# Performance work log

Measured on AMD Instinct MI355X. Metric: run time of the kernel, lower is better.

The kernel has to match this reference:

```python
import jax, jax.numpy as jnp
import numpy as np

N = 50000          # nodes
E = 800000         # directed edges (before self-loops)
NUM_CLASSES = 10
NEG_SLOPE = 0.2    # PyG GATConv default leaky_relu slope


def segment_softmax(logits, seg, num_segments):
    # numerically stable softmax over edges grouped by target node
    m = jax.ops.segment_max(logits, seg, num_segments=num_segments)
    e = jnp.exp(logits - m[seg])
    s = jax.ops.segment_sum(e, seg, num_segments=num_segments)
    return e / s[seg]


def gat_conv(x, src, dst, W, a_src, a_dst, b, n_nodes):
    # single-head PyG-style GATConv (eval mode: attention dropout disabled)
    h = x @ W                              # [N, C]
    alpha_src = h @ a_src                  # [N]
    alpha_dst = h @ a_dst                  # [N]
    logits = jax.nn.leaky_relu(alpha_src[src] + alpha_dst[dst], NEG_SLOPE)  # [E']
    alpha = segment_softmax(logits, dst, n_nodes)                            # [E']
    out = jax.ops.segment_sum(h[src] * alpha[:, None], dst, num_segments=n_nodes)
    return out + b


def setup_inputs() -> dict:
    key = jax.random.key(0)
    ks = jax.random.split(key, 13)
    x = jax.random.normal(ks[0], (N, 11), dtype=jnp.float32)
    edge_index = jax.random.randint(ks[1], (2, E), 0, N, dtype=jnp.int32)
    batch = jnp.zeros((N,), dtype=jnp.int32)  # unused by forward (no pooling)
    s = 0.1
    W1 = jax.random.normal(ks[2], (11, 16), jnp.float32) * s
    a1_src = jax.random.normal(ks[3], (16,), jnp.float32) * s
    a1_dst = jax.random.normal(ks[4], (16,), jnp.float32) * s
    b1 = jnp.zeros((16,), jnp.float32)
    W2 = jax.random.normal(ks[5], (16, 64), jnp.float32) * s
    a2_src = jax.random.normal(ks[6], (64,), jnp.float32) * s
    a2_dst = jax.random.normal(ks[7], (64,), jnp.float32) * s
    b2 = jnp.zeros((64,), jnp.float32)
    Wl = jax.random.normal(ks[8], (64, NUM_CLASSES), jnp.float32) * s
    bl = jnp.zeros((NUM_CLASSES,), jnp.float32)
    return {"x": x, "edge_index": edge_index, "batch": batch,
            "W1": W1, "a1_src": a1_src, "a1_dst": a1_dst, "b1": b1,
            "W2": W2, "a2_src": a2_src, "a2_dst": a2_dst, "b2": b2,
            "Wl": Wl, "bl": bl}


def reference(x, edge_index, batch, W1, a1_src, a1_dst, b1,
              W2, a2_src, a2_dst, b2, Wl, bl):
    n = x.shape[0]
    loop = jnp.arange(n, dtype=edge_index.dtype)
    src = jnp.concatenate([edge_index[0], loop])  # add self-loops (PyG default)
    dst = jnp.concatenate([edge_index[1], loop])
    h = gat_conv(x, src, dst, W1, a1_src, a1_dst, b1, n)
    h = jax.nn.relu(h)
    h = gat_conv(h, src, dst, W2, a2_src, a2_dst, b2, n)
    return h @ Wl + bl
```

## Files before the change

kernel.cpp:

```cpp
#include <hip/hip_runtime.h>
#include <hip/hip_bf16.h>
#include <hip/hip_fp16.h>

#define NEG_SLOPE 0.2f
#define BUCK 128
#define BSTRIDE 4096
#define SRCM 0x1FFFFFFu
#define SCH 2048

__device__ __forceinline__ float lrelu(float x) {
    return x > 0.f ? x : NEG_SLOPE * x;
}

__global__ __launch_bounds__(256)
void front_kernel(const float* __restrict__ x,
                  const float* __restrict__ W1,
                  const float* __restrict__ a1s, const float* __restrict__ a1d,
                  __half* __restrict__ h, float* __restrict__ as, float* __restrict__ ad,
                  int n, int tb,
                  const float* __restrict__ W2,
                  const float* __restrict__ a2s, const float* __restrict__ a2d,
                  const float* __restrict__ b2,
                  const float* __restrict__ Wl, const float* __restrict__ bl,
                  float* __restrict__ va, float* __restrict__ vd,
                  float* __restrict__ Wc, float* __restrict__ bc,
                  int* __restrict__ gcur, int nbuck) {
    const int bid = blockIdx.x;
    if (bid < tb) {
        constexpr int F_IN = 11, C_OUT = 16;
        __shared__ float sW[F_IN * C_OUT];
        __shared__ float sAs[C_OUT];
        __shared__ float sAd[C_OUT];
        for (int i = threadIdx.x; i < F_IN * C_OUT; i += 256) sW[i] = W1[i];
        if (threadIdx.x < C_OUT) { sAs[threadIdx.x] = a1s[threadIdx.x]; sAd[threadIdx.x] = a1d[threadIdx.x]; }
        __syncthreads();
        int i = bid * 256 + threadIdx.x;
        if (i >= n) return;
        float xin[F_IN];
#pragma unroll
        for (int f = 0; f < F_IN; ++f) xin[f] = x[(size_t)i * F_IN + f];
        float r[C_OUT];
        float s_acc = 0.f, d_acc = 0.f;
#pragma unroll
        for (int c = 0; c < C_OUT; ++c) {
            float acc = 0.f;
#pragma unroll
            for (int f = 0; f < F_IN; ++f) acc = fmaf(xin[f], sW[f * C_OUT + c], acc);
            r[c] = acc;
            s_acc = fmaf(acc, sAs[c], s_acc);
            d_acc = fmaf(acc, sAd[c], d_acc);
        }
        unsigned int u[8];
#pragma unroll
        for (int k = 0; k < 8; ++k) {
            __half2 hh = __floats2half2_rn(r[2 * k], r[2 * k + 1]);
            u[k] = *reinterpret_cast<unsigned int*>(&hh);
        }
        uint4* hp = reinterpret_cast<uint4*>(&h[(size_t)i * 16]);
        hp[0] = make_uint4(u[0], u[1], u[2], u[3]);
        hp[1] = make_uint4(u[4], u[5], u[6], u[7]);
        as[i] = s_acc;
        ad[i] = d_acc;
    } else {
        int t = threadIdx.x;
        for (int i = t; i < nbuck; i += 256) gcur[i] = i * BSTRIDE;
        if (t < 16) {
            float s = 0.f, s2 = 0.f;
            for (int c = 0; c < 64; ++c) {
                float w = W2[t * 64 + c];
                s = fmaf(w, a2s[c], s);
                s2 = fmaf(w, a2d[c], s2);
            }
            va[t] = s; vd[t] = s2;
        }
        int i = t - 64;
        if (i >= 0 && i < 160) {
            int f = i / 10, k = i % 10;
            float s = 0.f;
            for (int c = 0; c < 64; ++c) s = fmaf(W2[f * 64 + c], Wl[c * 10 + k], s);
            Wc[i] = s;
        }
        int k2 = t - 240;
        if (k2 >= 0 && k2 < 10) {
            float s = bl[k2];
            for (int c = 0; c < 64; ++c) s = fmaf(b2[c], Wl[c * 10 + k2], s);
            bc[k2] = s;
        }
    }
}

__global__ __launch_bounds__(256)
void scatter_kernel(const int* __restrict__ ei, int E, int ET,
                    int* __restrict__ gcur, uint2* __restrict__ pk, int nbuck,
                    const float* __restrict__ as1, const float* __restrict__ ad1) {
    __shared__ int lhist[512];
    for (int i = threadIdx.x; i < nbuck; i += 256) lhist[i] = 0;
    __syncthreads();
    const int tid = threadIdx.x;
    const int beg = blockIdx.x * SCH;

    int rs0, rs1, rs2, rs3, rs4, rs5, rs6, rs7;
    int rd0, rd1, rd2, rd3, rd4, rd5, rd6, rd7;
    const int e0 = beg + tid * 4;
    const int e1 = e0 + 1024;
    if (e0 + 3 < E) {
        const int4 s4 = *reinterpret_cast<const int4*>(&ei[e0]);
        const int4 d4 = *reinterpret_cast<const int4*>(&ei[E + e0]);
        rs0 = s4.x; rs1 = s4.y; rs2 = s4.z; rs3 = s4.w;
        rd0 = d4.x; rd1 = d4.y; rd2 = d4.z; rd3 = d4.w;
    } else {
        rs0 = rd0 = (e0 + 0 < ET) ? ((e0 + 0 < E) ? 0 : e0 + 0 - E) : -1;
        if (e0 + 0 < E) { rs0 = ei[e0 + 0]; rd0 = ei[E + e0 + 0]; }
        rs1 = rd1 = (e0 + 1 < ET) ? ((e0 + 1 < E) ? 0 : e0 + 1 - E) : -1;
        if (e0 + 1 < E) { rs1 = ei[e0 + 1]; rd1 = ei[E + e0 + 1]; }
        rs2 = rd2 = (e0 + 2 < ET) ? ((e0 + 2 < E) ? 0 : e0 + 2 - E) : -1;
        if (e0 + 2 < E) { rs2 = ei[e0 + 2]; rd2 = ei[E + e0 + 2]; }
        rs3 = rd3 = (e0 + 3 < ET) ? ((e0 + 3 < E) ? 0 : e0 + 3 - E) : -1;
        if (e0 + 3 < E) { rs3 = ei[e0 + 3]; rd3 = ei[E + e0 + 3]; }
    }
    if (e1 + 3 < E) {
        const int4 s4 = *reinterpret_cast<const int4*>(&ei[e1]);
        const int4 d4 = *reinterpret_cast<const int4*>(&ei[E + e1]);
        rs4 = s4.x; rs5 = s4.y; rs6 = s4.z; rs7 = s4.w;
        rd4 = d4.x; rd5 = d4.y; rd6 = d4.z; rd7 = d4.w;
    } else {
        rs4 = rd4 = (e1 + 0 < ET) ? ((e1 + 0 < E) ? 0 : e1 + 0 - E) : -1;
        if (e1 + 0 < E) { rs4 = ei[e1 + 0]; rd4 = ei[E + e1 + 0]; }
        rs5 = rd5 = (e1 + 1 < ET) ? ((e1 + 1 < E) ? 0 : e1 + 1 - E) : -1;
        if (e1 + 1 < E) { rs5 = ei[e1 + 1]; rd5 = ei[E + e1 + 1]; }
        rs6 = rd6 = (e1 + 2 < ET) ? ((e1 + 2 < E) ? 0 : e1 + 2 - E) : -1;
        if (e1 + 2 < E) { rs6 = ei[e1 + 2]; rd6 = ei[E + e1 + 2]; }
        rs7 = rd7 = (e1 + 3 < ET) ? ((e1 + 3 < E) ? 0 : e1 + 3 - E) : -1;
        if (e1 + 3 < E) { rs7 = ei[e1 + 3]; rd7 = ei[E + e1 + 3]; }
    }

    if (rd0 >= 0) atomicAdd(&lhist[rd0 >> 7], 1);
    if (rd1 >= 0) atomicAdd(&lhist[rd1 >> 7], 1);
    if (rd2 >= 0) atomicAdd(&lhist[rd2 >> 7], 1);
    if (rd3 >= 0) atomicAdd(&lhist[rd3 >> 7], 1);
    if (rd4 >= 0) atomicAdd(&lhist[rd4 >> 7], 1);
    if (rd5 >= 0) atomicAdd(&lhist[rd5 >> 7], 1);
    if (rd6 >= 0) atomicAdd(&lhist[rd6 >> 7], 1);
    if (rd7 >= 0) atomicAdd(&lhist[rd7 >> 7], 1);
    __syncthreads();

    for (int i = threadIdx.x; i < nbuck; i += 256) {
        int c = lhist[i];
        lhist[i] = (c > 0) ? atomicAdd(&gcur[i], c) : 0;
    }
    __syncthreads();

#define EMIT(RS, RD)                                                                   \
    if (RD >= 0) {                                                                     \
        float w = __expf(lrelu(as1[RS] + ad1[RD]));                                    \
        int slot = atomicAdd(&lhist[RD >> 7], 1);                                      \
        pk[slot] = make_uint2(((unsigned int)(RD & 127) << 25) | (unsigned int)RS,     \
                              __float_as_uint(w));                                     \
    }
    EMIT(rs0, rd0) EMIT(rs1, rd1) EMIT(rs2, rd2) EMIT(rs3, rd3)
    EMIT(rs4, rd4) EMIT(rs5, rd5) EMIT(rs6, rd6) EMIT(rs7, rd7)
#undef EMIT
}

__global__ __launch_bounds__(256)
void bucketsort_kernel(const uint2* __restrict__ pk,
                       const int* __restrict__ gcur,
                       uint2* __restrict__ cw,
                       int* __restrict__ row_beg, int* __restrict__ deg,
                       int n) {
    __shared__ uint2 sbuf[BSTRIDE];
    __shared__ uint2 dbuf[BSTRIDE];
    __shared__ int lcnt[BUCK];
    __shared__ int lofs[BUCK];
    const int tid = threadIdx.x;
    const int base = blockIdx.x * BUCK;
    const int beg = blockIdx.x * BSTRIDE;
    const int cnt = gcur[blockIdx.x] - beg;

    if (tid < BUCK) lcnt[tid] = 0;
    for (int i = tid * 2; i < cnt; i += 512) {
        if (i + 1 < cnt) {
            *reinterpret_cast<uint4*>(&sbuf[i]) = *reinterpret_cast<const uint4*>(&pk[beg + i]);
        } else {
            sbuf[i] = pk[beg + i];
        }
    }
    __syncthreads();
    for (int i = tid; i < cnt; i += 256)
        atomicAdd(&lcnt[sbuf[i].x >> 25], 1);
    __syncthreads();
    int v = 0;
    if (tid < BUCK) { v = lcnt[tid]; lofs[tid] = v; }
    __syncthreads();
    for (int off = 1; off < BUCK; off <<= 1) {
        int u = 0;
        if (tid < BUCK && tid >= off) u = lofs[tid - off];
        __syncthreads();
        if (tid < BUCK && tid >= off) lofs[tid] += u;
        __syncthreads();
    }
    if (tid < BUCK) {
        int excl = lofs[tid] - v;
        if (base + tid < n) {
            row_beg[base + tid] = beg + excl;
            deg[base + tid] = v;
        }
        lcnt[tid] = excl;
    }
    __syncthreads();
    for (int i = tid; i < cnt; i += 256) {
        uint2 rec = sbuf[i];
        int slot = atomicAdd(&lcnt[rec.x >> 25], 1);
        dbuf[slot] = rec;
    }
    __syncthreads();
    for (int i = tid * 2; i < cnt; i += 512) {
        if (i + 1 < cnt) {
            *reinterpret_cast<uint4*>(&cw[beg + i]) = *reinterpret_cast<uint4*>(&dbuf[i]);
        } else {
            cw[beg + i] = dbuf[i];
        }
    }
}

__global__ void gat_agg1_kernel(const int* __restrict__ row_beg,
                                const int* __restrict__ deg,
                                const uint2* __restrict__ cw,
                                const __half* __restrict__ h,
                                const float* __restrict__ b1,
                                const float* __restrict__ va,
                                const float* __restrict__ vd,
                                __half* __restrict__ X1r,
                                float* __restrict__ as2,
                                float* __restrict__ ad2, int n) {
    __shared__ float sb1[16], sva[16], svd[16];
    if (threadIdx.x < 16) {
        sb1[threadIdx.x] = b1[threadIdx.x];
        sva[threadIdx.x] = va[threadIdx.x];
        svd[threadIdx.x] = vd[threadIdx.x];
    }
    __syncthreads();
    int node = (blockIdx.x * blockDim.x + threadIdx.x) >> 4;
    int sl = threadIdx.x & 15;
    if (node >= n) return;
    int beg = row_beg[node];
    int end = beg + deg[node];

    const int eq = sl >> 2;
    const int cl = sl & 3;
    float lsum = 0.f;
    float4 acc = {0.f, 0.f, 0.f, 0.f};
    for (int chunk = beg; chunk < end; chunk += 16) {
        int e = chunk + sl;
        float wv = 0.f; int sv = 0;
        if (e < end) {
            uint2 rec = cw[e];
            sv = (int)(rec.x & SRCM);
            wv = __uint_as_float(rec.y);
            lsum += wv;
        }
        const int nch = min(16, end - chunk);
        const int T = (nch + 3) >> 2;
        for (int t = 0; t < T; ++t) {
            int j = t * 4 + eq;
            float wj = __shfl(wv, j, 16);
            int   sj = __shfl(sv, j, 16);
            if (j < nch) {
                uint2 hv2 = *reinterpret_cast<const uint2*>(&h[(size_t)sj * 16 + cl * 4]);
                float2 f01 = __half22float2(*reinterpret_cast<__half2*>(&hv2.x));
                float2 f23 = __half22float2(*reinterpret_cast<__half2*>(&hv2.y));
                acc.x = fmaf(wj, f01.x, acc.x);
                acc.y = fmaf(wj, f01.y, acc.y);
                acc.z = fmaf(wj, f23.x, acc.z);
                acc.w = fmaf(wj, f23.y, acc.w);
            }
        }
    }
#pragma unroll
    for (int k = 1; k < 16; k <<= 1) lsum += __shfl_xor(lsum, k, 16);
#pragma unroll
    for (int k = 4; k < 16; k <<= 1) {
        acc.x += __shfl_xor(acc.x, k, 16);
        acc.y += __shfl_xor(acc.y, k, 16);
        acc.z += __shfl_xor(acc.z, k, 16);
        acc.w += __shfl_xor(acc.w, k, 16);
    }
    float inv = 1.f / lsum;
    float x0 = fmaxf(fmaf(acc.x, inv, sb1[cl * 4 + 0]), 0.f);
    float x1 = fmaxf(fmaf(acc.y, inv, sb1[cl * 4 + 1]), 0.f);
    float x2 = fmaxf(fmaf(acc.z, inv, sb1[cl * 4 + 2]), 0.f);
    float x3 = fmaxf(fmaf(acc.w, inv, sb1[cl * 4 + 3]), 0.f);
    if (eq == 0) {
        __half2 p01 = __floats2half2_rn(x0, x1);
        __half2 p23 = __floats2half2_rn(x2, x3);
        uint2 o = make_uint2(*reinterpret_cast<unsigned int*>(&p01),
                             *reinterpret_cast<unsigned int*>(&p23));
        *reinterpret_cast<uint2*>(&X1r[(size_t)node * 16 + cl * 4]) = o;
    }
    float p = x0 * sva[cl * 4] + x1 * sva[cl * 4 + 1] + x2 * sva[cl * 4 + 2] + x3 * sva[cl * 4 + 3];
    float q = x0 * svd[cl * 4] + x1 * svd[cl * 4 + 1] + x2 * svd[cl * 4 + 2] + x3 * svd[cl * 4 + 3];
    p += __shfl_xor(p, 1, 16); p += __shfl_xor(p, 2, 16);
    q += __shfl_xor(q, 1, 16); q += __shfl_xor(q, 2, 16);
    if (sl == 0) { as2[node] = p; ad2[node] = q; }
}

__global__ void gat_agg2_kernel(const int* __restrict__ row_beg,
                                const int* __restrict__ deg,
                                const uint2* __restrict__ cw,
                                const float* __restrict__ as2,
                                const float* __restrict__ ad2,
                                const __half* __restrict__ X1r,
                                const float* __restrict__ Wc,
                                const float* __restrict__ bc,
                                float* __restrict__ out, int n) {
    __shared__ float sWc[160], sbc[10];
    for (int i = threadIdx.x; i < 160; i += blockDim.x) sWc[i] = Wc[i];
    if (threadIdx.x < 10) sbc[threadIdx.x] = bc[threadIdx.x];
    __syncthreads();
    int node = (blockIdx.x * blockDim.x + threadIdx.x) >> 4;
    int sl = threadIdx.x & 15;
    if (node >= n) return;
    int beg = row_beg[node];
    int end = beg + deg[node];
    float add = ad2[node];

    const int eq = sl >> 2;
    const int cl = sl & 3;
    float lsum = 0.f;
    float4 acc = {0.f, 0.f, 0.f, 0.f};
    for (int chunk = beg; chunk < end; chunk += 16) {
        int e = chunk + sl;
        float wv = 0.f; int sv = 0;
        if (e < end) {
            sv = (int)(cw[e].x & SRCM);
            wv = __expf(lrelu(as2[sv] + add));
            lsum += wv;
        }
        const int nch = min(16, end - chunk);
        const int T = (nch + 3) >> 2;
        for (int t = 0; t < T; ++t) {
            int j = t * 4 + eq;
            float wj = __shfl(wv, j, 16);
            int   sj = __shfl(sv, j, 16);
            if (j < nch) {
                uint2 hv2 = *reinterpret_cast<const uint2*>(&X1r[(size_t)sj * 16 + cl * 4]);
                float2 f01 = __half22float2(*reinterpret_cast<__half2*>(&hv2.x));
                float2 f23 = __half22float2(*reinterpret_cast<__half2*>(&hv2.y));
                acc.x = fmaf(wj, f01.x, acc.x);
                acc.y = fmaf(wj, f01.y, acc.y);
                acc.z = fmaf(wj, f23.x, acc.z);
                acc.w = fmaf(wj, f23.y, acc.w);
            }
        }
    }
#pragma unroll
    for (int k = 1; k < 16; k <<= 1) lsum += __shfl_xor(lsum, k, 16);
#pragma unroll
    for (int k = 4; k < 16; k <<= 1) {
        acc.x += __shfl_xor(acc.x, k, 16);
        acc.y += __shfl_xor(acc.y, k, 16);
        acc.z += __shfl_xor(acc.z, k, 16);
        acc.w += __shfl_xor(acc.w, k, 16);
    }
    float inv = 1.f / lsum;
    acc.x *= inv; acc.y *= inv; acc.z *= inv; acc.w *= inv;
    float p[10];
#pragma unroll
    for (int k = 0; k < 10; ++k) {
        p[k] = acc.x * sWc[(cl * 4 + 0) * 10 + k]
             + acc.y * sWc[(cl * 4 + 1) * 10 + k]
             + acc.z * sWc[(cl * 4 + 2) * 10 + k]
             + acc.w * sWc[(cl * 4 + 3) * 10 + k];
    }
#pragma unroll
    for (int k = 0; k < 10; ++k) {
        p[k] += __shfl_xor(p[k], 1, 16);
        p[k] += __shfl_xor(p[k], 2, 16);
    }
    if (sl < 10) {
        float v = p[0];
#pragma unroll
        for (int k = 1; k < 10; ++k) v = (sl == k) ? p[k] : v;
        out[(size_t)node * 10 + sl] = v + sbc[sl];
    }
}

extern "C" void kernel_launch(void* const* d_in, const int* in_sizes, int n_in,
                              void* d_out, int out_size, void* d_ws, size_t ws_size,
                              hipStream_t stream) {
    const float* x       = (const float*)d_in[0];
    const int*   ei      = (const int*)d_in[1];
    const float* W1      = (const float*)d_in[3];
    const float* a1_src  = (const float*)d_in[4];
    const float* a1_dst  = (const float*)d_in[5];
    const float* b1      = (const float*)d_in[6];
    const float* W2      = (const float*)d_in[7];
    const float* a2_src  = (const float*)d_in[8];
    const float* a2_dst  = (const float*)d_in[9];
    const float* b2      = (const float*)d_in[10];
    const float* Wl      = (const float*)d_in[11];
    const float* bl      = (const float*)d_in[12];
    float* out = (float*)d_out;

    const int N = in_sizes[2];
    const int E = in_sizes[1] / 2;
    const int ET = E + N;

    const int B = 256;
    auto cdiv = [](int a, int b) { return (a + b - 1) / b; };

    const int NBUCK = cdiv(N, BUCK);
    const int NBLK  = cdiv(ET, SCH);
    const int TB    = cdiv(N, B);

    char* ws = (char*)d_ws;
    size_t off = 0;
    auto alloc = [&](size_t bytes) {
        char* p = ws + off;
        off = (off + bytes + 255) & ~(size_t)255;
        return p;
    };
    __half*       h1   = (__half*)alloc((size_t)N * 16 * 2);
    __half*       X1r  = (__half*)alloc((size_t)N * 16 * 2);
    float*        as1  = (float*)alloc((size_t)N * 4);
    float*        ad1  = (float*)alloc((size_t)N * 4);
    float*        as2  = (float*)alloc((size_t)N * 4);
    float*        ad2  = (float*)alloc((size_t)N * 4);
    int*          rowb = (int*)alloc((size_t)N * 4);
    int*          degb = (int*)alloc((size_t)N * 4);
    uint2*        cw   = (uint2*)alloc((size_t)NBUCK * BSTRIDE * 8);
    uint2*        pk   = (uint2*)alloc((size_t)NBUCK * BSTRIDE * 8);
    int*          gcur = (int*)alloc((size_t)NBUCK * 4);
    float*        va   = (float*)alloc(16 * 4);
    float*        vd   = (float*)alloc(16 * 4);
    float*        Wc   = (float*)alloc(160 * 4);
    float*        bc   = (float*)alloc(10 * 4);
    (void)ws_size;

    front_kernel<<<TB + 1, B, 0, stream>>>(
        x, W1, a1_src, a1_dst, h1, as1, ad1, N, TB,
        W2, a2_src, a2_dst, b2, Wl, bl, va, vd, Wc, bc, gcur, NBUCK);

    scatter_kernel<<<NBLK, B, 0, stream>>>(ei, E, ET, gcur, pk, NBUCK, as1, ad1);

    bucketsort_kernel<<<NBUCK, 256, 0, stream>>>(pk, gcur, cw, rowb, degb, N);

    gat_agg1_kernel<<<cdiv(N * 16, B), B, 0, stream>>>(rowb, degb, cw, h1, b1, va, vd, X1r, as2, ad2, N);

    gat_agg2_kernel<<<cdiv(N * 16, B), B, 0, stream>>>(rowb, degb, cw, as2, ad2, X1r, Wc, bc, out, N);
}
```

Measured before the change: 67.59 us.

## Fuse bucket sort with layer-1 aggregation and widen feature loads to 16B

Merges the bucket sort kernel and the first GAT aggregation into one kernel. Each block sorts its bucket in shared memory through a 16-bit index permutation instead of a second record buffer, then aggregates its 128 nodes straight from shared memory, so the layer-1 pass no longer re-reads sorted edges from global memory and one launch goes away. Both aggregation kernels now split the 16 lanes into 8 edge-lanes by 2 channel-lanes with 16-byte half-precision loads, which raises per-lane load width and lowers shuffle-reduction depth. In exchange, only 256 threads per bucket block do the layer-1 aggregation, so that phase has less parallelism and may be less able to hide gather latency.

After: 73.66 us. 9.0% more time.

```diff
diff --git a/kernel.cpp b/kernel.cpp
--- a/kernel.cpp
+++ b/kernel.cpp
@@ -163,20 +163,28 @@
 }
 
 __global__ __launch_bounds__(256)
-void bucketsort_kernel(const uint2* __restrict__ pk,
-                       const int* __restrict__ gcur,
-                       uint2* __restrict__ cw,
-                       int* __restrict__ row_beg, int* __restrict__ deg,
-                       int n) {
-    __shared__ uint2 sbuf[BSTRIDE];
-    __shared__ uint2 dbuf[BSTRIDE];
+void sortagg1_kernel(const uint2* __restrict__ pk,
+                     const int* __restrict__ gcur,
+                     uint2* __restrict__ cw,
+                     int* __restrict__ row_beg, int* __restrict__ deg,
+                     const __half* __restrict__ h,
+                     const float* __restrict__ b1,
+                     const float* __restrict__ va,
+                     const float* __restrict__ vd,
+                     __half* __restrict__ X1r,
+                     float* __restrict__ as2,
+                     float* __restrict__ ad2, int n) {
+    __shared__ __align__(16) uint2 sbuf[BSTRIDE];
+    __shared__ unsigned short sidx[BSTRIDE];
     __shared__ int lcnt[BUCK];
     __shared__ int lofs[BUCK];
+    __shared__ float sb1[16], sva[16], svd[16];
     const int tid = threadIdx.x;
     const int base = blockIdx.x * BUCK;
     const int beg = blockIdx.x * BSTRIDE;
     const int cnt = gcur[blockIdx.x] - beg;
 
+    if (tid < 16) { sb1[tid] = b1[tid]; sva[tid] = va[tid]; svd[tid] = vd[tid]; }
     if (tid < BUCK) lcnt[tid] = 0;
     for (int i = tid * 2; i < cnt; i += 512) {
         if (i + 1 < cnt) {
@@ -206,102 +214,93 @@
             deg[base + tid] = v;
         }
         lcnt[tid] = excl;
+        lofs[tid] = excl;
     }
     __syncthreads();
     for (int i = tid; i < cnt; i += 256) {
-        uint2 rec = sbuf[i];
-        int slot = atomicAdd(&lcnt[rec.x >> 25], 1);
-        dbuf[slot] = rec;
-    }
-    __syncthreads();
-    for (int i = tid * 2; i < cnt; i += 512) {
-        if (i + 1 < cnt) {
-            *reinterpret_cast<uint4*>(&cw[beg + i]) = *reinterpret_cast<uint4*>(&dbuf[i]);
-        } else {
-            cw[beg + i] = dbuf[i];
-        }
-    }
-}
-
-__global__ void gat_agg1_kernel(const int* __restrict__ row_beg,
-                                const int* __restrict__ deg,
-                                const uint2* __restrict__ cw,
-                                const __half* __restrict__ h,
-                                const float* __restrict__ b1,
-                                const float* __restrict__ va,
-                                const float* __restrict__ vd,
-                                __half* __restrict__ X1r,
-                                float* __restrict__ as2,
-                                float* __restrict__ ad2, int n) {
-    __shared__ float sb1[16], sva[16], svd[16];
-    if (threadIdx.x < 16) {
-        sb1[threadIdx.x] = b1[threadIdx.x];
-        sva[threadIdx.x] = va[threadIdx.x];
-        svd[threadIdx.x] = vd[threadIdx.x];
-    }
-    __syncthreads();
-    int node = (blockIdx.x * blockDim.x + threadIdx.x) >> 4;
-    int sl = threadIdx.x & 15;
-    if (node >= n) return;
-    int beg = row_beg[node];
-    int end = beg + deg[node];
-
-    const int eq = sl >> 2;
-    const int cl = sl & 3;
-    float lsum = 0.f;
-    float4 acc = {0.f, 0.f, 0.f, 0.f};
-    for (int chunk = beg; chunk < end; chunk += 16) {
-        int e = chunk + sl;
-        float wv = 0.f; int sv = 0;
-        if (e < end) {
-            uint2 rec = cw[e];
-            sv = (int)(rec.x & SRCM);
-            wv = __uint_as_float(rec.y);
-            lsum += wv;
-        }
-        const int nch = min(16, end - chunk);
-        const int T = (nch + 3) >> 2;
-        for (int t = 0; t < T; ++t) {
-            int j = t * 4 + eq;
-            float wj = __shfl(wv, j, 16);
-            int   sj = __shfl(sv, j, 16);
-            if (j < nch) {
-                uint2 hv2 = *reinterpret_cast<const uint2*>(&h[(size_t)sj * 16 + cl * 4]);
-                float2 f01 = __half22float2(*reinterpret_cast<__half2*>(&hv2.x));
-                float2 f23 = __half22float2(*reinterpret_cast<__half2*>(&hv2.y));
-                acc.x = fmaf(wj, f01.x, acc.x);
-                acc.y = fmaf(wj, f01.y, acc.y);
-                acc.z = fmaf(wj, f23.x, acc.z);
-                acc.w = fmaf(wj, f23.y, acc.w);
+        int d = (int)(sbuf[i].x >> 25);
+        int slot = atomicAdd(&lcnt[d], 1);
+        sidx[slot] = (unsigned short)i;
+    }
+    __syncthreads();
+    for (int j = tid; j < cnt; j += 256) cw[beg + j] = sbuf[sidx[j]];
+
+    const int sg = tid >> 4;
+    const int sl = tid & 15;
+    const int eq = sl >> 1;
+    const int cl = sl & 1;
+    for (int r = 0; r < BUCK / 16; ++r) {
+        int l = r * 16 + sg;
+        int node = base + l;
+        int nbeg = lofs[l];
+        int ndeg = lcnt[l] - nbeg;
+        float lsum = 0.f;
+        float a0 = 0.f, a1 = 0.f, a2 = 0.f, a3 = 0.f, a4 = 0.f, a5 = 0.f, a6 = 0.f, a7 = 0.f;
+        for (int chunk = 0; chunk < ndeg; chunk += 16) {
+            int e = chunk + sl;
+            float wv = 0.f; int sv = 0;
+            if (e < ndeg) {
+                uint2 rec = sbuf[sidx[nbeg + e]];
+                sv = (int)(rec.x & SRCM);
+                wv = __uint_as_float(rec.y);
+                lsum += wv;
             }
-        }
-    }
-#pragma unroll
-    for (int k = 1; k < 16; k <<= 1) lsum += __shfl_xor(lsum, k, 16);
-#pragma unroll
-    for (int k = 4; k < 16; k <<= 1) {
-        acc.x += __shfl_xor(acc.x, k, 16);
-        acc.y += __shfl_xor(acc.y, k, 16);
-        acc.z += __shfl_xor(acc.z, k, 16);
-        acc.w += __shfl_xor(acc.w, k, 16);
-    }
-    float inv = 1.f / lsum;
-    float x0 = fmaxf(fmaf(acc.x, inv, sb1[cl * 4 + 0]), 0.f);
-    float x1 = fmaxf(fmaf(acc.y, inv, sb1[cl * 4 + 1]), 0.f);
-    float x2 = fmaxf(fmaf(acc.z, inv, sb1[cl * 4 + 2]), 0.f);
-    float x3 = fmaxf(fmaf(acc.w, inv, sb1[cl * 4 + 3]), 0.f);
-    if (eq == 0) {
-        __half2 p01 = __floats2half2_rn(x0, x1);
-        __half2 p23 = __floats2half2_rn(x2, x3);
-        uint2 o = make_uint2(*reinterpret_cast<unsigned int*>(&p01),
-                             *reinterpret_cast<unsigned int*>(&p23));
-        *reinterpret_cast<uint2*>(&X1r[(size_t)node * 16 + cl * 4]) = o;
-    }
-    float p = x0 * sva[cl * 4] + x1 * sva[cl * 4 + 1] + x2 * sva[cl * 4 + 2] + x3 * sva[cl * 4 + 3];
-    float q = x0 * svd[cl * 4] + x1 * svd[cl * 4 + 1] + x2 * svd[cl * 4 + 2] + x3 * svd[cl * 4 + 3];
-    p += __shfl_xor(p, 1, 16); p += __shfl_xor(p, 2, 16);
-    q += __shfl_xor(q, 1, 16); q += __shfl_xor(q, 2, 16);
-    if (sl == 0) { as2[node] = p; ad2[node] = q; }
+            const int nch = min(16, ndeg - chunk);
+            const int T = (nch + 7) >> 3;
+            for (int t = 0; t < T; ++t) {
+                int j = t * 8 + eq;
+                float wj = __shfl(wv, j, 16);
+                int   sj = __shfl(sv, j, 16);
+                if (j < nch) {
+                    uint4 hv = *reinterpret_cast<const uint4*>(&h[(size_t)sj * 16 + cl * 8]);
+                    float2 f0 = __half22float2(*reinterpret_cast<__half2*>(&hv.x));
+                    float2 f1 = __half22float2(*reinterpret_cast<__half2*>(&hv.y));
+                    float2 f2 = __half22float2(*reinterpret_cast<__half2*>(&hv.z));
+                    float2 f3 = __half22float2(*reinterpret_cast<__half2*>(&hv.w));
+                    a0 = fmaf(wj, f0.x, a0); a1 = fmaf(wj, f0.y, a1);
+                    a2 = fmaf(wj, f1.x, a2); a3 = fmaf(wj, f1.y, a3);
+                    a4 = fmaf(wj, f2.x, a4); a5 = fmaf(wj, f2.y, a5);
+                    a6 = fmaf(wj, f3.x, a6); a7 = fmaf(wj, f3.y, a7);
+                }
+            }
+        }
+#pragma unroll
+        for (int k = 1; k < 16; k <<= 1) lsum += __shfl_xor(lsum, k, 16);
+#pragma unroll
+        for (int k = 2; k < 16; k <<= 1) {
+            a0 += __shfl_xor(a0, k, 16); a1 += __shfl_xor(a1, k, 16);
+            a2 += __shfl_xor(a2, k, 16); a3 += __shfl_xor(a3, k, 16);
+            a4 += __shfl_xor(a4, k, 16); a5 += __shfl_xor(a5, k, 16);
+            a6 += __shfl_xor(a6, k, 16); a7 += __shfl_xor(a7, k, 16);
+        }
+        float inv = 1.f / lsum;
+        float x0 = fmaxf(fmaf(a0, inv, sb1[cl * 8 + 0]), 0.f);
+        float x1 = fmaxf(fmaf(a1, inv, sb1[cl * 8 + 1]), 0.f);
+        float x2 = fmaxf(fmaf(a2, inv, sb1[cl * 8 + 2]), 0.f);
+        float x3 = fmaxf(fmaf(a3, inv, sb1[cl * 8 + 3]), 0.f);
+        float x4 = fmaxf(fmaf(a4, inv, sb1[cl * 8 + 4]), 0.f);
+        float x5 = fmaxf(fmaf(a5, inv, sb1[cl * 8 + 5]), 0.f);
+        float x6 = fmaxf(fmaf(a6, inv, sb1[cl * 8 + 6]), 0.f);
+        float x7 = fmaxf(fmaf(a7, inv, sb1[cl * 8 + 7]), 0.f);
+        if (eq == 0 && node < n) {
+            __half2 p01 = __floats2half2_rn(x0, x1);
+            __half2 p23 = __floats2half2_rn(x2, x3);
+            __half2 p45 = __floats2half2_rn(x4, x5);
+            __half2 p67 = __floats2half2_rn(x6, x7);
+            uint4 o = make_uint4(*reinterpret_cast<unsigned int*>(&p01),
+                                 *reinterpret_cast<unsigned int*>(&p23),
+                                 *reinterpret_cast<unsigned int*>(&p45),
+                                 *reinterpret_cast<unsigned int*>(&p67));
+            *reinterpret_cast<uint4*>(&X1r[(size_t)node * 16 + cl * 8]) = o;
+        }
+        float p = x0 * sva[cl * 8 + 0] + x1 * sva[cl * 8 + 1] + x2 * sva[cl * 8 + 2] + x3 * sva[cl * 8 + 3]
+                + x4 * sva[cl * 8 + 4] + x5 * sva[cl * 8 + 5] + x6 * sva[cl * 8 + 6] + x7 * sva[cl * 8 + 7];
+        float q = x0 * svd[cl * 8 + 0] + x1 * svd[cl * 8 + 1] + x2 * svd[cl * 8 + 2] + x3 * svd[cl * 8 + 3]
+                + x4 * svd[cl * 8 + 4] + x5 * svd[cl * 8 + 5] + x6 * svd[cl * 8 + 6] + x7 * svd[cl * 8 + 7];
+        p += __shfl_xor(p, 1, 16);
+        q += __shfl_xor(q, 1, 16);
+        if (sl == 0 && node < n) { as2[node] = p; ad2[node] = q; }
+    }
 }
 
 __global__ void gat_agg2_kernel(const int* __restrict__ row_beg,
@@ -324,10 +323,10 @@
     int end = beg + deg[node];
     float add = ad2[node];
 
-    const int eq = sl >> 2;
-    const int cl = sl & 3;
+    const int eq = sl >> 1;
+    const int cl = sl & 1;
     float lsum = 0.f;
-    float4 acc = {0.f, 0.f, 0.f, 0.f};
+    float a0 = 0.f, a1 = 0.f, a2 = 0.f, a3 = 0.f, a4 = 0.f, a5 = 0.f, a6 = 0.f, a7 = 0.f;
     for (int chunk = beg; chunk < end; chunk += 16) {
         int e = chunk + sl;
         float wv = 0.f; int sv = 0;
@@ -337,46 +336,46 @@
             lsum += wv;
         }
         const int nch = min(16, end - chunk);
-        const int T = (nch + 3) >> 2;
+        const int T = (nch + 7) >> 3;
         for (int t = 0; t < T; ++t) {
-            int j = t * 4 + eq;
+            int j = t * 8 + eq;
             float wj = __shfl(wv, j, 16);
             int   sj = __shfl(sv, j, 16);
             if (j < nch) {
-                uint2 hv2 = *reinterpret_cast<const uint2*>(&X1r[(size_t)sj * 16 + cl * 4]);
-                float2 f01 = __half22float2(*reinterpret_cast<__half2*>(&hv2.x));
-                float2 f23 = __half22float2(*reinterpret_cast<__half2*>(&hv2.y));
-                acc.x = fmaf(wj, f01.x, acc.x);
-                acc.y = fmaf(wj, f01.y, acc.y);
-                acc.z = fmaf(wj, f23.x, acc.z);
-                acc.w = fmaf(wj, f23.y, acc.w);
+                uint4 hv = *reinterpret_cast<const uint4*>(&X1r[(size_t)sj * 16 + cl * 8]);
+                float2 f0 = __half22float2(*reinterpret_cast<__half2*>(&hv.x));
+                float2 f1 = __half22float2(*reinterpret_cast<__half2*>(&hv.y));
+                float2 f2 = __half22float2(*reinterpret_cast<__half2*>(&hv.z));
+                float2 f3 = __half22float2(*reinterpret_cast<__half2*>(&hv.w));
+                a0 = fmaf(wj, f0.x, a0); a1 = fmaf(wj, f0.y, a1);
+                a2 = fmaf(wj, f1.x, a2); a3 = fmaf(wj, f1.y, a3);
+                a4 = fmaf(wj, f2.x, a4); a5 = fmaf(wj, f2.y, a5);
+                a6 = fmaf(wj, f3.x, a6); a7 = fmaf(wj, f3.y, a7);
             }
         }
     }
 #pragma unroll
     for (int k = 1; k < 16; k <<= 1) lsum += __shfl_xor(lsum, k, 16);
 #pragma unroll
-    for (int k = 4; k < 16; k <<= 1) {
-        acc.x += __shfl_xor(acc.x, k, 16);
-        acc.y += __shfl_xor(acc.y, k, 16);
-        acc.z += __shfl_xor(acc.z, k, 16);
-        acc.w += __shfl_xor(acc.w, k, 16);
+    for (int k = 2; k < 16; k <<= 1) {
+        a0 += __shfl_xor(a0, k, 16); a1 += __shfl_xor(a1, k, 16);
+        a2 += __shfl_xor(a2, k, 16); a3 += __shfl_xor(a3, k, 16);
+        a4 += __shfl_xor(a4, k, 16); a5 += __shfl_xor(a5, k, 16);
+        a6 += __shfl_xor(a6, k, 16); a7 += __shfl_xor(a7, k, 16);
     }
     float inv = 1.f / lsum;
-    acc.x *= inv; acc.y *= inv; acc.z *= inv; acc.w *= inv;
+    a0 *= inv; a1 *= inv; a2 *= inv; a3 *= inv;
+    a4 *= inv; a5 *= inv; a6 *= inv; a7 *= inv;
     float p[10];
 #pragma unroll
     for (int k = 0; k < 10; ++k) {
-        p[k] = acc.x * sWc[(cl * 4 + 0) * 10 + k]
-             + acc.y * sWc[(cl * 4 + 1) * 10 + k]
-             + acc.z * sWc[(cl * 4 + 2) * 10 + k]
-             + acc.w * sWc[(cl * 4 + 3) * 10 + k];
-    }
-#pragma unroll
-    for (int k = 0; k < 10; ++k) {
-        p[k] += __shfl_xor(p[k], 1, 16);
-        p[k] += __shfl_xor(p[k], 2, 16);
-    }
+        p[k] = a0 * sWc[(cl * 8 + 0) * 10 + k] + a1 * sWc[(cl * 8 + 1) * 10 + k]
+             + a2 * sWc[(cl * 8 + 2) * 10 + k] + a3 * sWc[(cl * 8 + 3) * 10 + k]
+             + a4 * sWc[(cl * 8 + 4) * 10 + k] + a5 * sWc[(cl * 8 + 5) * 10 + k]
+             + a6 * sWc[(cl * 8 + 6) * 10 + k] + a7 * sWc[(cl * 8 + 7) * 10 + k];
+    }
+#pragma unroll
+    for (int k = 0; k < 10; ++k) p[k] += __shfl_xor(p[k], 1, 16);
     if (sl < 10) {
         float v = p[0];
 #pragma unroll
@@ -443,9 +442,8 @@
 
     scatter_kernel<<<NBLK, B, 0, stream>>>(ei, E, ET, gcur, pk, NBUCK, as1, ad1);
 
-    bucketsort_kernel<<<NBUCK, 256, 0, stream>>>(pk, gcur, cw, rowb, degb, N);
-
-    gat_agg1_kernel<<<cdiv(N * 16, B), B, 0, stream>>>(rowb, degb, cw, h1, b1, va, vd, X1r, as2, ad2, N);
+    sortagg1_kernel<<<NBUCK, 256, 0, stream>>>(pk, gcur, cw, rowb, degb,
+                                               h1, b1, va, vd, X1r, as2, ad2, N);
 
     gat_agg2_kernel<<<cdiv(N * 16, B), B, 0, stream>>>(rowb, degb, cw, as2, ad2, X1r, Wc, bc, out, N);
 }
```
